# Kernel tuning notes

Measured on AMD Instinct MI355X. Metric: run time of the kernel, lower is better.

The kernel has to match this reference:

```python
import jax, jax.numpy as jnp
import numpy as np

B, L1, L2 = 128, 256, 256
EMBED, HIDDEN, OUT = 512, 1024, 3


def _mlp(x, w1, b1, w2, b2):
    # MLPLayer (dropout is identity in eval): ReLU(ReLU(x W1^T + b1) W2^T + b2)
    h = jax.nn.relu(x @ w1.T + b1)
    return jax.nn.relu(h @ w2.T + b2)


def setup_inputs() -> dict:
    key = jax.random.key(0)
    ks = jax.random.split(key, 18)
    s = 0.05
    inp = {
        'sent1': jax.random.normal(ks[0], (B, L1, EMBED), jnp.float32),
        'sent2': jax.random.normal(ks[1], (B, L2, EMBED), jnp.float32),
        # attend MLP f: embed -> hidden -> hidden
        'f_w1': jax.random.normal(ks[2], (HIDDEN, EMBED), jnp.float32) * s,
        'f_b1': jnp.zeros((HIDDEN,), jnp.float32),
        'f_w2': jax.random.normal(ks[3], (HIDDEN, HIDDEN), jnp.float32) * s,
        'f_b2': jnp.zeros((HIDDEN,), jnp.float32),
        # compare MLP g: 2*embed -> hidden -> hidden
        'g_w1': jax.random.normal(ks[4], (HIDDEN, 2 * EMBED), jnp.float32) * s,
        'g_b1': jnp.zeros((HIDDEN,), jnp.float32),
        'g_w2': jax.random.normal(ks[5], (HIDDEN, HIDDEN), jnp.float32) * s,
        'g_b2': jnp.zeros((HIDDEN,), jnp.float32),
        # aggregate MLP h: 2*hidden -> hidden -> hidden
        'h_w1': jax.random.normal(ks[6], (HIDDEN, 2 * HIDDEN), jnp.float32) * s,
        'h_b1': jnp.zeros((HIDDEN,), jnp.float32),
        'h_w2': jax.random.normal(ks[7], (HIDDEN, HIDDEN), jnp.float32) * s,
        'h_b2': jnp.zeros((HIDDEN,), jnp.float32),
        # final linear: hidden -> out
        'fin_w': jax.random.normal(ks[8], (OUT, HIDDEN), jnp.float32) * s,
        'fin_b': jnp.zeros((OUT,), jnp.float32),
    }
    return inp


def reference(sent1, sent2, f_w1, f_b1, f_w2, f_b2, g_w1, g_b1, g_w2, g_b2,
              h_w1, h_b1, h_w2, h_b2, fin_w, fin_b):
    # ---- Attend ----
    f1 = _mlp(sent1, f_w1, f_b1, f_w2, f_b2)            # [B, L1, H]
    f2 = _mlp(sent2, f_w1, f_b1, f_w2, f_b2)            # [B, L2, H]
    e1 = jnp.einsum('bih,bjh->bij', f1, f2)             # [B, L1, L2], no scaling
    w1a = jax.nn.softmax(e1, axis=-1)                    # softmax over L2
    w2a = jax.nn.softmax(jnp.swapaxes(e1, 1, 2), axis=-1)  # [B, L2, L1], softmax over L1
    att1 = jnp.einsum('bij,bje->bie', w1a, sent2)       # [B, L1, E]
    att2 = jnp.einsum('bji,bie->bje', w2a, sent1)       # [B, L2, E]
    # ---- Compare ----
    cmp1 = _mlp(jnp.concatenate([att1, sent1], axis=2), g_w1, g_b1, g_w2, g_b2)  # [B, L1, H]
    cmp2 = _mlp(jnp.concatenate([att2, sent2], axis=2), g_w1, g_b1, g_w2, g_b2)  # [B, L2, H]
    # ---- Aggregate ----
    s1 = jnp.sum(cmp1, axis=1)                          # [B, H]
    s2 = jnp.sum(cmp2, axis=1)                          # [B, H]
    h = _mlp(jnp.concatenate([s1, s2], axis=1), h_w1, h_b1, h_w2, h_b2)
    return h @ fin_w.T + fin_b                          # [B, OUT]
```

## Files before the change

### kernel.cpp

```cpp
#include <hip/hip_runtime.h>
#include <hip/hip_bf16.h>


using f32x4 = __attribute__((ext_vector_type(4))) float;
using s16x8 = __attribute__((ext_vector_type(8))) short;

__device__ __forceinline__ void gload_lds16(const short* g, short* l) {
  __builtin_amdgcn_global_load_lds(
      (const __attribute__((address_space(1))) unsigned int*)g,
      (__attribute__((address_space(3))) unsigned int*)l, 16, 0, 0);
}

template <bool RELU, bool OUT_BF16, bool HAS_BIAS, bool SUML, bool CONCAT>
__global__ __launch_bounds__(256, 4) void gemm_nt(
    const short* __restrict__ A, const short* __restrict__ B,
    const float* __restrict__ bias, void* __restrict__ Cv, int K, int lda,
    int ldb, int ldc, long sA, long sB, long sC, const float* __restrict__ cs1,
    const float* __restrict__ cs2, int cBh) {
  __shared__ __align__(16) short As[128 * 64];
  __shared__ __align__(16) short Bs[128 * 64];
  const int t = threadIdx.x;
  const int lane = t & 63;
  const int wave = t >> 6;

  unsigned flat = (blockIdx.z * gridDim.y + blockIdx.y) * gridDim.x + blockIdx.x;
  const unsigned total = gridDim.x * gridDim.y * gridDim.z;
  unsigned bx = blockIdx.x, by = blockIdx.y, bz = blockIdx.z;
  if ((total & 7u) == 0) {
    unsigned nf = (flat & 7u) * (total >> 3) + (flat >> 3);
    bx = nf % gridDim.x;
    unsigned rest = nf / gridDim.x;
    by = rest % gridDim.y;
    bz = rest / gridDim.y;
  }
  const int m0 = by * 128;
  const int n0 = bx * 128;
  const long zb = bz;

  const int srow = t >> 3;
  const int schunk = ((t & 7) ^ (srow & 7)) * 8;
  const short* ag = A + zb * sA + (long)(m0 + srow) * lda + schunk;
  const short* bg = B + zb * sB + (long)(n0 + srow) * ldb + schunk;
  const long a32 = (long)32 * lda, b32 = (long)32 * ldb;
  short* AsW = As + wave * 512;
  short* BsW = Bs + wave * 512;

  const int fr = lane & 15;
  const int kq = lane >> 4;
  int aoff[4], boff[4];
#pragma unroll
  for (int i = 0; i < 4; ++i) {
    const int ra = (wave >> 1) * 64 + i * 16 + fr;
    const int rb = (wave & 1) * 64 + i * 16 + fr;
    aoff[i] = ra * 64 + ((kq ^ (ra & 7)) * 8);
    boff[i] = rb * 64 + ((kq ^ (rb & 7)) * 8);
  }

  f32x4 acc[4][4] = {};

  for (int it = K >> 6; it > 0; --it) {
    gload_lds16(ag, AsW);
    gload_lds16(ag + a32, AsW + 2048);
    gload_lds16(ag + 2 * a32, AsW + 4096);
    gload_lds16(ag + 3 * a32, AsW + 6144);
    gload_lds16(bg, BsW);
    gload_lds16(bg + b32, BsW + 2048);
    gload_lds16(bg + 2 * b32, BsW + 4096);
    gload_lds16(bg + 3 * b32, BsW + 6144);
    ag += 64;
    bg += 64;
    __syncthreads();
#pragma unroll
    for (int kk = 0; kk < 2; ++kk) {
      const int x = kk * 32;
      s16x8 af[4], bfv[4];
#pragma unroll
      for (int i = 0; i < 4; ++i) af[i] = *(const s16x8*)(As + (aoff[i] ^ x));
#pragma unroll
      for (int j = 0; j < 4; ++j) bfv[j] = *(const s16x8*)(Bs + (boff[j] ^ x));
#pragma unroll
      for (int i = 0; i < 4; ++i)
#pragma unroll
        for (int j = 0; j < 4; ++j)
          acc[i][j] = __builtin_amdgcn_mfma_f32_16x16x32_bf16(
              af[i], bfv[j], acc[i][j], 0, 0, 0);
    }
    __syncthreads();
  }

  const int ccol = lane & 15;
  const int crow = (lane >> 4) * 4;

  if constexpr (SUML) {
    __shared__ float ssum[128];
    if (t < 128) ssum[t] = 0.f;
    __syncthreads();
#pragma unroll
    for (int j = 0; j < 4; ++j) {
      const int lcol = (wave & 1) * 64 + j * 16 + ccol;
      float bj = HAS_BIAS ? bias[n0 + lcol] : 0.f;
      float part = 0.f;
#pragma unroll
      for (int i = 0; i < 4; ++i)
#pragma unroll
        for (int r = 0; r < 4; ++r) {
          float x = acc[i][j][r] + bj;
          if (RELU) x = fmaxf(x, 0.f);
          part += x;
        }
      atomicAdd(&ssum[lcol], part);
    }
    __syncthreads();
    if (t < 128) {
      const int split = (int)sC;
      int rb2 = m0 >> 8;
      const int side = rb2 >= split;
      rb2 -= side * split;
      atomicAdd((float*)Cv + (long)rb2 * ldc + side * (ldc >> 1) + n0 + t,
                ssum[t]);
    }
  } else {
#pragma unroll
    for (int j = 0; j < 4; ++j) {
      const int col = n0 + (wave & 1) * 64 + j * 16 + ccol;
      float bj = 0.f;
      if (HAS_BIAS) bj = bias[col];
#pragma unroll
      for (int i = 0; i < 4; ++i) {
        const int row0 = m0 + (wave >> 1) * 64 + i * 16 + crow;
#pragma unroll
        for (int r = 0; r < 4; ++r) {
          float x = acc[i][j][r] + bj;
          if (RELU) x = fmaxf(x, 0.f);
          const long idx = (long)(row0 + r) * ldc + col + zb * sC;
          if (OUT_BF16)
            ((__hip_bfloat16*)Cv)[idx] = __float2bfloat16(x);
          else
            ((float*)Cv)[idx] = x;
        }
      }
    }
    if constexpr (CONCAT) {
      const int side = (int)(zb >= (long)cBh);
      const int bb = (int)zb - side * cBh;
      const float* csrc = side ? cs2 : cs1;
      const long crowbase = (long)bb * 256;
      __hip_bfloat16* Cb = (__hip_bfloat16*)Cv + zb * sC + 512 + n0;
#pragma unroll
      for (int k = 0; k < 16; ++k) {
        const int idx = k * 256 + t;
        const int r = idx >> 5;
        const int q = idx & 31;
        const float4 v =
            *(const float4*)(csrc + (crowbase + m0 + r) * 512 + n0 + q * 4);
        union {
          ushort4 u;
          __hip_bfloat16 h[4];
        } pk;
        pk.h[0] = __float2bfloat16(v.x);
        pk.h[1] = __float2bfloat16(v.y);
        pk.h[2] = __float2bfloat16(v.z);
        pk.h[3] = __float2bfloat16(v.w);
        *(ushort4*)(Cb + (long)(m0 + r) * ldc + q * 4) = pk.u;
      }
    }
  }
}

struct CastArgs {
  const float* src[6];
  __hip_bfloat16* dst[6];
  long n[6];
};
__global__ void cast_many(CastArgs a) {
  const int w = blockIdx.y;
  long i = ((long)blockIdx.x * blockDim.x + threadIdx.x) * 4;
  if (i >= a.n[w]) return;
  float4 v = *(const float4*)(a.src[w] + i);
  __hip_bfloat16* o = a.dst[w] + i;
  o[0] = __float2bfloat16(v.x);
  o[1] = __float2bfloat16(v.y);
  o[2] = __float2bfloat16(v.z);
  o[3] = __float2bfloat16(v.w);
}

__global__ void cast_bf16(const float* __restrict__ in,
                          __hip_bfloat16* __restrict__ out, long n) {
  long i = ((long)blockIdx.x * blockDim.x + threadIdx.x) * 4;
  if (i >= n) return;
  float4 v = *(const float4*)(in + i);
  out[i + 0] = __float2bfloat16(v.x);
  out[i + 1] = __float2bfloat16(v.y);
  out[i + 2] = __float2bfloat16(v.z);
  out[i + 3] = __float2bfloat16(v.w);
}

__global__ void prep_sent(const float* __restrict__ s1,
                          const float* __restrict__ s2,
                          __hip_bfloat16* __restrict__ S12b,
                          __hip_bfloat16* __restrict__ STbase, int Bh) {
  __shared__ float tile[32][33];
  const int z = blockIdx.z;
  const int e0 = blockIdx.x * 32;
  const int l0 = blockIdx.y * 32;
  const int side = z >= Bh;
  const int b = z - side * Bh;
  const float* ib = (side ? s2 : s1) + (long)b * 131072;
  __hip_bfloat16* on = S12b + (long)z * 131072;
  __hip_bfloat16* ot = STbase + (long)(side ? b : (Bh + b)) * 131072;
  const int tx = threadIdx.x, ty = threadIdx.y;
#pragma unroll
  for (int k = 0; k < 4; ++k) {
    const int l = l0 + ty + 8 * k;
    const float v = ib[(long)l * 512 + e0 + tx];
    on[(long)l * 512 + e0 + tx] = __float2bfloat16(v);
    tile[ty + 8 * k][tx] = v;
  }
  __syncthreads();
#pragma unroll
  for (int k = 0; k < 4; ++k)
    ot[(long)(e0 + ty + 8 * k) * 256 + l0 + tx] =
        __float2bfloat16(tile[tx][ty + 8 * k]);
}

__global__ void softmax_rows(const float* __restrict__ E,
                             __hip_bfloat16* __restrict__ W) {
  const long row = blockIdx.x;
  const int t = threadIdx.x;
  const float x = E[row * 256 + t];
  float m = x;
  for (int o = 32; o > 0; o >>= 1) m = fmaxf(m, __shfl_xor(m, o));
  __shared__ float red[4];
  if ((t & 63) == 0) red[t >> 6] = m;
  __syncthreads();
  m = fmaxf(fmaxf(red[0], red[1]), fmaxf(red[2], red[3]));
  const float pr = __expf(x - m);
  float s = pr;
  for (int o = 32; o > 0; o >>= 1) s += __shfl_xor(s, o);
  __shared__ float red2[4];
  if ((t & 63) == 0) red2[t >> 6] = s;
  __syncthreads();
  s = red2[0] + red2[1] + red2[2] + red2[3];
  W[row * 256 + t] = __float2bfloat16(pr / s);
}

__global__ __launch_bounds__(256) void softmax_cols_f(
    const float* __restrict__ E, __hip_bfloat16* __restrict__ W) {
  __shared__ float tile[256][65];
  __shared__ float mred[4][64], sred[4][64];
  const int b = blockIdx.y;
  const int j0 = blockIdx.x * 64;
  const int t = threadIdx.x;
  const int jl = t & 63, s = t >> 6;
  const float* Eb = E + (long)b * 65536 + j0;
#pragma unroll
  for (int k = 0; k < 64; ++k) {
    const int i = k * 4 + s;
    tile[i][jl] = Eb[(long)i * 256 + jl];
  }
  __syncthreads();
  float m = -3.4e38f;
#pragma unroll 8
  for (int r = 0; r < 64; ++r) m = fmaxf(m, tile[s * 64 + r][jl]);
  mred[s][jl] = m;
  __syncthreads();
  m = fmaxf(fmaxf(mred[0][jl], mred[1][jl]), fmaxf(mred[2][jl], mred[3][jl]));
  float sum = 0.f;
#pragma unroll 8
  for (int r = 0; r < 64; ++r) sum += __expf(tile[s * 64 + r][jl] - m);
  sred[s][jl] = sum;
  __syncthreads();
  const int jw = t >> 2;
  const int ib = t & 3;
  const float mj = fmaxf(fmaxf(mred[0][jw], mred[1][jw]),
                         fmaxf(mred[2][jw], mred[3][jw]));
  const float isj =
      1.0f / (sred[0][jw] + sred[1][jw] + sred[2][jw] + sred[3][jw]);
  __hip_bfloat16* Wb = W + (long)b * 65536 + (long)(j0 + jw) * 256 + ib * 64;
#pragma unroll 8
  for (int r = 0; r < 64; ++r)
    Wb[r] = __float2bfloat16(__expf(tile[ib * 64 + r][jw] - mj) * isj);
}

__global__ void final_lin(const __hip_bfloat16* __restrict__ h2,
                          const float* __restrict__ w,
                          const float* __restrict__ bs,
                          float* __restrict__ out) {
  const int b = blockIdx.x;
  const int t = threadIdx.x;
  float p0 = 0.f, p1 = 0.f, p2 = 0.f;
  for (int k = t; k < 1024; k += 256) {
    const float x = __bfloat162float(h2[(long)b * 1024 + k]);
    p0 += x * w[k];
    p1 += x * w[1024 + k];
    p2 += x * w[2048 + k];
  }
  for (int o = 32; o > 0; o >>= 1) {
    p0 += __shfl_xor(p0, o);
    p1 += __shfl_xor(p1, o);
    p2 += __shfl_xor(p2, o);
  }
  __shared__ float r[4][3];
  if ((t & 63) == 0) {
    r[t >> 6][0] = p0;
    r[t >> 6][1] = p1;
    r[t >> 6][2] = p2;
  }
  __syncthreads();
  if (t < 3)
    out[b * 3 + t] = r[0][t] + r[1][t] + r[2][t] + r[3][t] + bs[t];
}

extern "C" void kernel_launch(void* const* d_in, const int* in_sizes, int n_in,
                              void* d_out, int out_size, void* d_ws,
                              size_t ws_size, hipStream_t stream) {
  const float* sent1 = (const float*)d_in[0];
  const float* sent2 = (const float*)d_in[1];
  const float* f_w1 = (const float*)d_in[2];
  const float* f_b1 = (const float*)d_in[3];
  const float* f_w2 = (const float*)d_in[4];
  const float* f_b2 = (const float*)d_in[5];
  const float* g_w1 = (const float*)d_in[6];
  const float* g_b1 = (const float*)d_in[7];
  const float* g_w2 = (const float*)d_in[8];
  const float* g_b2 = (const float*)d_in[9];
  const float* h_w1 = (const float*)d_in[10];
  const float* h_b1 = (const float*)d_in[11];
  const float* h_w2 = (const float*)d_in[12];
  const float* h_b2 = (const float*)d_in[13];
  const float* fin_w = (const float*)d_in[14];
  const float* fin_b = (const float*)d_in[15];

  char* p = (char*)d_ws;
  auto take = [&](size_t n) {
    char* r = p;
    p += (n + 255) & ~(size_t)255;
    return r;
  };
  const int Bh = (ws_size >= (size_t)220 * 1024 * 1024) ? 64 : 32;
  const int chunks = 128 / Bh;
  const long R = (long)Bh * 256;

  short* Wf1 = (short*)take(1024L * 512 * 2);
  short* Wf2 = (short*)take(1024L * 1024 * 2);
  short* Wg1 = (short*)take(1024L * 1024 * 2);
  short* Wg2 = (short*)take(1024L * 1024 * 2);
  short* Wh1 = (short*)take(1024L * 2048 * 2);
  short* Wh2 = (short*)take(1024L * 1024 * 2);
  float* SUMF = (float*)take(128L * 2048 * 4);
  short* scat = (short*)take(128L * 2048 * 2);
  short* hh = (short*)take(128L * 1024 * 2);
  short* hf = (short*)take(128L * 1024 * 2);
  char* Areg = take(2 * R * 1024 * 2);
  char* Breg = take(2 * R * 1024 * 2);
  char* Creg = take(2 * R * 512 * 2);
  char* Dreg = take(2 * R * 512 * 2);
  (void)in_sizes; (void)n_in; (void)out_size;

  short* FHID = (short*)Areg;
  short* GHID = (short*)Areg;
  short* F12 = (short*)Breg;
  short* CC12 = (short*)Breg;
  short* S12b = (short*)Creg;
  float* E1 = (float*)Creg;
  short* W1A = (short*)(Creg + (long)Bh * 262144);
  short* W2A = W1A + (long)Bh * 65536;
  short* ST = (short*)Dreg;

  hipMemsetAsync(SUMF, 0, 128L * 2048 * 4, stream);

  CastArgs ca;
  ca.src[0] = f_w1; ca.dst[0] = (__hip_bfloat16*)Wf1; ca.n[0] = 524288;
  ca.src[1] = f_w2; ca.dst[1] = (__hip_bfloat16*)Wf2; ca.n[1] = 1048576;
  ca.src[2] = g_w1; ca.dst[2] = (__hip_bfloat16*)Wg1; ca.n[2] = 1048576;
  ca.src[3] = g_w2; ca.dst[3] = (__hip_bfloat16*)Wg2; ca.n[3] = 1048576;
  ca.src[4] = h_w1; ca.dst[4] = (__hip_bfloat16*)Wh1; ca.n[4] = 2097152;
  ca.src[5] = h_w2; ca.dst[5] = (__hip_bfloat16*)Wh2; ca.n[5] = 1048576;
  cast_many<<<dim3(2048, 6), 256, 0, stream>>>(ca);

  for (int c = 0; c < chunks; ++c) {
    const float* s1 = sent1 + (long)c * R * 512;
    const float* s2 = sent2 + (long)c * R * 512;
    float* SUMF_c = SUMF + (long)c * Bh * 2048;
    const int MT = (int)(2 * R / 128);

    prep_sent<<<dim3(16, 8, 2 * Bh), dim3(32, 8), 0, stream>>>(
        s1, s2, (__hip_bfloat16*)S12b, (__hip_bfloat16*)ST, Bh);

    gemm_nt<true, true, true, false, false><<<dim3(8, MT, 1), 256, 0, stream>>>(
        S12b, Wf1, f_b1, FHID, 512, 512, 512, 1024, 0, 0, 0, nullptr, nullptr, 0);
    gemm_nt<true, true, true, false, false><<<dim3(8, MT, 1), 256, 0, stream>>>(
        FHID, Wf2, f_b2, F12, 1024, 1024, 1024, 1024, 0, 0, 0, nullptr, nullptr, 0);

    gemm_nt<false, false, false, false, false><<<dim3(2, 2, Bh), 256, 0, stream>>>(
        F12, F12 + R * 1024, nullptr, E1, 1024, 1024, 1024, 256, 256L * 1024,
        256L * 1024, 65536, nullptr, nullptr, 0);

    softmax_rows<<<Bh * 256, 256, 0, stream>>>(E1, (__hip_bfloat16*)W1A);
    softmax_cols_f<<<dim3(4, Bh), 256, 0, stream>>>(E1, (__hip_bfloat16*)W2A);

    gemm_nt<false, true, false, false, true><<<dim3(4, 2, 2 * Bh), 256, 0, stream>>>(
        W1A, ST, nullptr, CC12, 256, 256, 256, 1024, 65536, 131072, 262144,
        s1, s2, Bh);

    gemm_nt<true, true, true, false, false><<<dim3(8, MT, 1), 256, 0, stream>>>(
        CC12, Wg1, g_b1, GHID, 1024, 1024, 1024, 1024, 0, 0, 0, nullptr, nullptr, 0);
    gemm_nt<true, false, true, true, false><<<dim3(8, MT, 1), 256, 0, stream>>>(
        GHID, Wg2, g_b2, SUMF_c, 1024, 1024, 1024, 2048, 0, 0, Bh, nullptr, nullptr, 0);
  }

  cast_bf16<<<256, 256, 0, stream>>>(SUMF, (__hip_bfloat16*)scat, 262144);
  gemm_nt<true, true, true, false, false><<<dim3(8, 1, 1), 256, 0, stream>>>(
      scat, Wh1, h_b1, hh, 2048, 2048, 2048, 1024, 0, 0, 0, nullptr, nullptr, 0);
  gemm_nt<true, true, true, false, false><<<dim3(8, 1, 1), 256, 0, stream>>>(
      hh, Wh2, h_b2, hf, 1024, 1024, 1024, 1024, 0, 0, 0, nullptr, nullptr, 0);
  final_lin<<<128, 256, 0, stream>>>((__hip_bfloat16*)hf, fin_w, fin_b,
                                     (float*)d_out);
}
```

Measured before the change: 922.4 us.

## Switch GEMM to 32x32x16 MFMA and add templated N-tile width

Replaces the 16x16x32 bf16 MFMA inner loop with 32x32x16 MFMA tiles, which cuts LDS fragment reads per FLOP and changes the accumulator and epilogue layout. It also makes the N tile width a template parameter, so the small batched GEMMs and the aggregate MLP GEMMs run with 64-wide tiles and more blocks. The aim is higher MFMA throughput and better occupancy on the undersized launches. The new epilogue row mapping has to match the 32x32 output layout exactly, which adds correctness risk.

```diff
diff --git a/kernel.cpp b/kernel.cpp
--- a/kernel.cpp
+++ b/kernel.cpp
@@ -3,6 +3,7 @@
 
 
 using f32x4 = __attribute__((ext_vector_type(4))) float;
+using f32x16 = __attribute__((ext_vector_type(16))) float;
 using s16x8 = __attribute__((ext_vector_type(8))) short;
 
 __device__ __forceinline__ void gload_lds16(const short* g, short* l) {
@@ -11,14 +12,16 @@
       (__attribute__((address_space(3))) unsigned int*)l, 16, 0, 0);
 }
 
-template <bool RELU, bool OUT_BF16, bool HAS_BIAS, bool SUML, bool CONCAT>
+template <int BN, bool RELU, bool OUT_BF16, bool HAS_BIAS, bool SUML,
+          bool CONCAT>
 __global__ __launch_bounds__(256, 4) void gemm_nt(
     const short* __restrict__ A, const short* __restrict__ B,
     const float* __restrict__ bias, void* __restrict__ Cv, int K, int lda,
     int ldb, int ldc, long sA, long sB, long sC, const float* __restrict__ cs1,
     const float* __restrict__ cs2, int cBh) {
+  constexpr int NH = BN / 64;
   __shared__ __align__(16) short As[128 * 64];
-  __shared__ __align__(16) short Bs[128 * 64];
+  __shared__ __align__(16) short Bs[BN * 64];
   const int t = threadIdx.x;
   const int lane = t & 63;
   const int wave = t >> 6;
@@ -34,7 +37,7 @@
     bz = rest / gridDim.y;
   }
   const int m0 = by * 128;
-  const int n0 = bx * 128;
+  const int n0 = bx * BN;
   const long zb = bz;
 
   const int srow = t >> 3;
@@ -45,65 +48,68 @@
   short* AsW = As + wave * 512;
   short* BsW = Bs + wave * 512;
 
-  const int fr = lane & 15;
-  const int kq = lane >> 4;
-  int aoff[4], boff[4];
-#pragma unroll
-  for (int i = 0; i < 4; ++i) {
-    const int ra = (wave >> 1) * 64 + i * 16 + fr;
-    const int rb = (wave & 1) * 64 + i * 16 + fr;
-    aoff[i] = ra * 64 + ((kq ^ (ra & 7)) * 8);
-    boff[i] = rb * 64 + ((kq ^ (rb & 7)) * 8);
-  }
-
-  f32x4 acc[4][4] = {};
+  const int ln = lane & 31;
+  const int hi = lane >> 5;
+  int abase[2], asw[2], bbase[NH], bsw[NH];
+#pragma unroll
+  for (int i = 0; i < 2; ++i) {
+    const int ra = (wave >> 1) * 64 + i * 32 + ln;
+    abase[i] = ra * 64;
+    asw[i] = ra & 7;
+  }
+#pragma unroll
+  for (int j = 0; j < NH; ++j) {
+    const int rb = (wave & 1) * (BN / 2) + j * 32 + ln;
+    bbase[j] = rb * 64;
+    bsw[j] = rb & 7;
+  }
+
+  f32x16 acc[2][NH] = {};
 
   for (int it = K >> 6; it > 0; --it) {
     gload_lds16(ag, AsW);
     gload_lds16(ag + a32, AsW + 2048);
     gload_lds16(ag + 2 * a32, AsW + 4096);
     gload_lds16(ag + 3 * a32, AsW + 6144);
-    gload_lds16(bg, BsW);
-    gload_lds16(bg + b32, BsW + 2048);
-    gload_lds16(bg + 2 * b32, BsW + 4096);
-    gload_lds16(bg + 3 * b32, BsW + 6144);
+#pragma unroll
+    for (int q = 0; q < BN / 32; ++q)
+      gload_lds16(bg + q * b32, BsW + q * 2048);
     ag += 64;
     bg += 64;
     __syncthreads();
 #pragma unroll
-    for (int kk = 0; kk < 2; ++kk) {
-      const int x = kk * 32;
-      s16x8 af[4], bfv[4];
-#pragma unroll
-      for (int i = 0; i < 4; ++i) af[i] = *(const s16x8*)(As + (aoff[i] ^ x));
-#pragma unroll
-      for (int j = 0; j < 4; ++j) bfv[j] = *(const s16x8*)(Bs + (boff[j] ^ x));
-#pragma unroll
-      for (int i = 0; i < 4; ++i)
-#pragma unroll
-        for (int j = 0; j < 4; ++j)
-          acc[i][j] = __builtin_amdgcn_mfma_f32_16x16x32_bf16(
+    for (int s = 0; s < 4; ++s) {
+      const int c = (s << 1) | hi;
+      s16x8 af[2], bfv[NH];
+#pragma unroll
+      for (int i = 0; i < 2; ++i)
+        af[i] = *(const s16x8*)(As + abase[i] + (((c ^ asw[i])) << 3));
+#pragma unroll
+      for (int j = 0; j < NH; ++j)
+        bfv[j] = *(const s16x8*)(Bs + bbase[j] + (((c ^ bsw[j])) << 3));
+#pragma unroll
+      for (int i = 0; i < 2; ++i)
+#pragma unroll
+        for (int j = 0; j < NH; ++j)
+          acc[i][j] = __builtin_amdgcn_mfma_f32_32x32x16_bf16(
               af[i], bfv[j], acc[i][j], 0, 0, 0);
     }
     __syncthreads();
   }
 
-  const int ccol = lane & 15;
-  const int crow = (lane >> 4) * 4;
-
   if constexpr (SUML) {
-    __shared__ float ssum[128];
-    if (t < 128) ssum[t] = 0.f;
+    __shared__ float ssum[BN];
+    if (t < BN) ssum[t] = 0.f;
     __syncthreads();
 #pragma unroll
-    for (int j = 0; j < 4; ++j) {
-      const int lcol = (wave & 1) * 64 + j * 16 + ccol;
+    for (int j = 0; j < NH; ++j) {
+      const int lcol = (wave & 1) * (BN / 2) + j * 32 + ln;
       float bj = HAS_BIAS ? bias[n0 + lcol] : 0.f;
       float part = 0.f;
 #pragma unroll
-      for (int i = 0; i < 4; ++i)
-#pragma unroll
-        for (int r = 0; r < 4; ++r) {
+      for (int i = 0; i < 2; ++i)
+#pragma unroll
+        for (int r = 0; r < 16; ++r) {
           float x = acc[i][j][r] + bj;
           if (RELU) x = fmaxf(x, 0.f);
           part += x;
@@ -111,7 +117,7 @@
       atomicAdd(&ssum[lcol], part);
     }
     __syncthreads();
-    if (t < 128) {
+    if (t < BN) {
       const int split = (int)sC;
       int rb2 = m0 >> 8;
       const int side = rb2 >= split;
@@ -121,18 +127,19 @@
     }
   } else {
 #pragma unroll
-    for (int j = 0; j < 4; ++j) {
-      const int col = n0 + (wave & 1) * 64 + j * 16 + ccol;
+    for (int j = 0; j < NH; ++j) {
+      const int col = n0 + (wave & 1) * (BN / 2) + j * 32 + ln;
       float bj = 0.f;
       if (HAS_BIAS) bj = bias[col];
 #pragma unroll
-      for (int i = 0; i < 4; ++i) {
-        const int row0 = m0 + (wave >> 1) * 64 + i * 16 + crow;
-#pragma unroll
-        for (int r = 0; r < 4; ++r) {
+      for (int i = 0; i < 2; ++i) {
+        const int rowb = m0 + (wave >> 1) * 64 + i * 32 + 4 * hi;
+#pragma unroll
+        for (int r = 0; r < 16; ++r) {
+          const int row = rowb + (r & 3) + 8 * (r >> 2);
           float x = acc[i][j][r] + bj;
           if (RELU) x = fmaxf(x, 0.f);
-          const long idx = (long)(row0 + r) * ldc + col + zb * sC;
+          const long idx = (long)row * ldc + col + zb * sC;
           if (OUT_BF16)
             ((__hip_bfloat16*)Cv)[idx] = __float2bfloat16(x);
           else
@@ -141,16 +148,17 @@
       }
     }
     if constexpr (CONCAT) {
+      constexpr int F4 = BN / 4;
       const int side = (int)(zb >= (long)cBh);
       const int bb = (int)zb - side * cBh;
       const float* csrc = side ? cs2 : cs1;
       const long crowbase = (long)bb * 256;
       __hip_bfloat16* Cb = (__hip_bfloat16*)Cv + zb * sC + 512 + n0;
 #pragma unroll
-      for (int k = 0; k < 16; ++k) {
+      for (int k = 0; k < BN / 8; ++k) {
         const int idx = k * 256 + t;
-        const int r = idx >> 5;
-        const int q = idx & 31;
+        const int r = idx / F4;
+        const int q = idx % F4;
         const float4 v =
             *(const float4*)(csrc + (crowbase + m0 + r) * 512 + n0 + q * 4);
         union {
@@ -387,32 +395,43 @@
     prep_sent<<<dim3(16, 8, 2 * Bh), dim3(32, 8), 0, stream>>>(
         s1, s2, (__hip_bfloat16*)S12b, (__hip_bfloat16*)ST, Bh);
 
-    gemm_nt<true, true, true, false, false><<<dim3(8, MT, 1), 256, 0, stream>>>(
-        S12b, Wf1, f_b1, FHID, 512, 512, 512, 1024, 0, 0, 0, nullptr, nullptr, 0);
-    gemm_nt<true, true, true, false, false><<<dim3(8, MT, 1), 256, 0, stream>>>(
-        FHID, Wf2, f_b2, F12, 1024, 1024, 1024, 1024, 0, 0, 0, nullptr, nullptr, 0);
-
-    gemm_nt<false, false, false, false, false><<<dim3(2, 2, Bh), 256, 0, stream>>>(
-        F12, F12 + R * 1024, nullptr, E1, 1024, 1024, 1024, 256, 256L * 1024,
-        256L * 1024, 65536, nullptr, nullptr, 0);
+    gemm_nt<128, true, true, true, false, false>
+        <<<dim3(8, MT, 1), 256, 0, stream>>>(S12b, Wf1, f_b1, FHID, 512, 512,
+                                             512, 1024, 0, 0, 0, nullptr,
+                                             nullptr, 0);
+    gemm_nt<128, true, true, true, false, false>
+        <<<dim3(8, MT, 1), 256, 0, stream>>>(FHID, Wf2, f_b2, F12, 1024, 1024,
+                                             1024, 1024, 0, 0, 0, nullptr,
+                                             nullptr, 0);
+
+    gemm_nt<64, false, false, false, false, false>
+        <<<dim3(4, 2, Bh), 256, 0, stream>>>(F12, F12 + R * 1024, nullptr, E1,
+                                             1024, 1024, 1024, 256, 256L * 1024,
+                                             256L * 1024, 65536, nullptr,
+                                             nullptr, 0);
 
     softmax_rows<<<Bh * 256, 256, 0, stream>>>(E1, (__hip_bfloat16*)W1A);
     softmax_cols_f<<<dim3(4, Bh), 256, 0, stream>>>(E1, (__hip_bfloat16*)W2A);
 
-    gemm_nt<false, true, false, false, true><<<dim3(4, 2, 2 * Bh), 256, 0, stream>>>(
-        W1A, ST, nullptr, CC12, 256, 256, 256, 1024, 65536, 131072, 262144,
-        s1, s2, Bh);
-
-    gemm_nt<true, true, true, false, false><<<dim3(8, MT, 1), 256, 0, stream>>>(
-        CC12, Wg1, g_b1, GHID, 1024, 1024, 1024, 1024, 0, 0, 0, nullptr, nullptr, 0);
-    gemm_nt<true, false, true, true, false><<<dim3(8, MT, 1), 256, 0, stream>>>(
-        GHID, Wg2, g_b2, SUMF_c, 1024, 1024, 1024, 2048, 0, 0, Bh, nullptr, nullptr, 0);
+    gemm_nt<64, false, true, false, false, true>
+        <<<dim3(8, 2, 2 * Bh), 256, 0, stream>>>(W1A, ST, nullptr, CC12, 256,
+                                                 256, 256, 1024, 65536, 131072,
+                                                 262144, s1, s2, Bh);
+
+    gemm_nt<128, true, true, true, false, false>
+        <<<dim3(8, MT, 1), 256, 0, stream>>>(CC12, Wg1, g_b1, GHID, 1024, 1024,
+                                             1024, 1024, 0, 0, 0, nullptr,
+                                             nullptr, 0);
+    gemm_nt<128, true, false, true, true, false>
+        <<<dim3(8, MT, 1), 256, 0, stream>>>(GHID, Wg2, g_b2, SUMF_c, 1024,
+                                             1024, 1024, 2048, 0, 0, Bh,
+                                             nullptr, nullptr, 0);
   }
 
   cast_bf16<<<256, 256, 0, stream>>>(SUMF, (__hip_bfloat16*)scat, 262144);
-  gemm_nt<true, true, true, false, false><<<dim3(8, 1, 1), 256, 0, stream>>>(
+  gemm_nt<64, true, true, true, false, false><<<dim3(16, 1, 1), 256, 0, stream>>>(
       scat, Wh1, h_b1, hh, 2048, 2048, 2048, 1024, 0, 0, 0, nullptr, nullptr, 0);
-  gemm_nt<true, true, true, false, false><<<dim3(8, 1, 1), 256, 0, stream>>>(
+  gemm_nt<64, true, true, true, false, false><<<dim3(16, 1, 1), 256, 0, stream>>>(
       hh, Wh2, h_b2, hf, 1024, 1024, 1024, 1024, 0, 0, 0, nullptr, nullptr, 0);
   final_lin<<<128, 256, 0, stream>>>((__hip_bfloat16*)hf, fin_w, fin_b,
                                      (float*)d_out);
```

New measurement: 983.8 us. 6.7% more time.
